# Performance work log

Measured on AMD Instinct MI355X. Metric: run time of the kernel, lower is better.

The kernel has to match this reference:

```python
import jax, jax.numpy as jnp
import numpy as np

T, TINI, N, P, M, B = 1500, 16, 32, 4, 4, 8192
LG = T - TINI - N + 1  # g dimension = 1453


def block_hankel(w, L, d):
    # w: flat signal of length T*d (row-major (T,d)); returns (L*d, T-L+1) block Hankel
    Tlen = w.shape[0] // d
    cols = Tlen - L + 1
    idx = jnp.arange(L * d)[:, None] + d * jnp.arange(cols)[None, :]
    return w[idx]


def setup_inputs():
    key = jax.random.key(0)
    ks = jax.random.split(key, 8)
    ud = jax.random.normal(ks[0], (T, M), jnp.float32)
    yd = jax.random.normal(ks[1], (T, P), jnp.float32)
    q = 100.0 + 0.01 * jax.random.normal(ks[2], (P,), jnp.float32)   # torch init: randn*0.01+100
    r = 0.01 + 0.001 * jax.random.normal(ks[3], (M,), jnp.float32)   # torch init: randn*0.001+0.01
    ref = jax.random.normal(ks[4], (B, N * P), jnp.float32)
    uref = jnp.zeros((B, N * M), jnp.float32)  # unused by forward math (matches torch)
    u_ini = jax.random.normal(ks[5], (B, TINI * M), jnp.float32)
    y_ini = jax.random.normal(ks[6], (B, TINI * P), jnp.float32)
    return dict(ref=ref, uref=uref, u_ini=u_ini, y_ini=y_ini, ud=ud, yd=yd, q=q, r=r)


def _forward(ref, u_ini, y_ini, ud, yd, q, r):
    # Hankel data matrices
    U = block_hankel(ud.reshape(-1), TINI + N, M)   # (M*(TINI+N), LG)
    Y = block_hankel(yd.reshape(-1), TINI + N, P)
    Up, Uf = U[: M * TINI], U[M * TINI :]           # (M*TINI, LG), (M*N, LG)
    Yp, Yf = Y[: P * TINI], Y[P * TINI :]

    # cost weights: Q_sqrt = diag(kron(ones(N), sqrt(q))) => squared weights tile(q, N)
    wq = jnp.tile(q, N)  # (N*P,)
    wr = jnp.tile(r, N)  # (N*M,)

    # QP in g: min g^T H g - 2 (Yf^T Wq ref)^T g  s.t.  A g = b
    H = Yf.T @ (wq[:, None] * Yf) + Uf.T @ (wr[:, None] * Uf)  # (LG, LG)
    A = jnp.concatenate([Up, Yp, Yf[-P:]], axis=0)             # equality constraints: Up g=u_ini, Yp g=y_ini, y[-P:]=ref[-P:]
    nc = A.shape[0]

    K = jnp.block([[2.0 * H, A.T], [A, jnp.zeros((nc, nc), H.dtype)]])  # KKT matrix (shared over batch)
    rhs = jnp.concatenate(
        [2.0 * (Yf.T @ (wq[:, None] * ref.T)), u_ini.T, y_ini.T, ref[:, -P:].T], axis=0
    )  # (LG+nc, B)

    sol = jnp.linalg.pinv(K) @ rhs   # min-norm KKT solution (K is singular: g non-unique, u/y unique)
    g = sol[:LG].T                   # (B, LG)
    u = g @ Uf.T                     # (B, N*M) optimal input
    y = g @ Yf.T                     # (B, N*P) optimal output
    return g, u, y


def reference(ref, uref, u_ini, y_ini, ud, yd, q, r):
    # uref is unused in the torch forward math as well (only a None-default placeholder)
    return _forward(ref, u_ini, y_ini, ud, yd, q, r)
```

## Files before the change

### kernel.cpp

```cpp
#include <hip/hip_runtime.h>

#define COLS_ 1453
#define NC 132
#define EGS 1792
#define NB 8192

#define oGam 0
#define oC   147456
#define oV   196608
#define oGC  213504
#define oCK  262656
#define oVK  311808
#define oGCK 328704
#define oB   377856
#define oP   410624
#define oR   414980
#define oJ   431364
#define oF   464132
#define oCE  496900

__device__ __forceinline__ double hash01(unsigned i, unsigned j) {
  unsigned x = i * 0x9E3779B9u ^ (j * 0x85EBCA6Bu + 0xC2B2AE35u);
  x ^= x >> 16; x *= 0x7FEB352Du; x ^= x >> 15; x *= 0x846CA68Bu; x ^= x >> 16;
  return (double)(x & 0xFFFFFF) / 8388608.0 - 1.0;
}

__global__ void k_gram(const float* __restrict__ ud, const float* __restrict__ yd,
                       double* __restrict__ G) {
  __shared__ float sig[12000];
  int tid = threadIdx.y * 16 + threadIdx.x;
  for (int idx = tid; idx < 6000; idx += 256) { sig[idx] = ud[idx]; sig[6000 + idx] = yd[idx]; }
  __syncthreads();
  int i = blockIdx.y * 16 + threadIdx.y;
  int j = blockIdx.x * 16 + threadIdx.x;
  const float* si = &sig[(i < 192) ? i : (6000 + i - 192)];
  const float* sj = &sig[(j < 192) ? j : (6000 + j - 192)];
  double a0 = 0.0, a1 = 0.0, a2 = 0.0, a3 = 0.0;
  for (int c = 0; c < 1452; c += 4) {
    a0 += (double)si[4 * c]      * (double)sj[4 * c];
    a1 += (double)si[4 * c + 4]  * (double)sj[4 * c + 4];
    a2 += (double)si[4 * c + 8]  * (double)sj[4 * c + 8];
    a3 += (double)si[4 * c + 12] * (double)sj[4 * c + 12];
  }
  a0 += (double)si[4 * 1452] * (double)sj[4 * 1452];
  G[i * 384 + j] = (a0 + a1) + (a2 + a3);
}

__global__ void k_initc(double* __restrict__ c, double* __restrict__ v) {
  int z = blockIdx.x * 16 + threadIdx.x;
  int i = blockIdx.y * 16 + threadIdx.y;
  if (i < 384) c[i * 128 + z] = hash01(i, z);
  else if (i < 516) v[(i - 384) * 128 + z] = hash01(i + 1000, z);
}

__global__ void k_G(const double* __restrict__ Gam, const double* __restrict__ c,
                    double* __restrict__ outp) {
  int z = blockIdx.x * 16 + threadIdx.x;
  int i = blockIdx.y * 16 + threadIdx.y;
  double a0 = 0.0, a1 = 0.0;
  for (int t = 0; t < 384; t += 2) {
    a0 += Gam[i * 384 + t]     * c[t * 128 + z];
    a1 += Gam[i * 384 + t + 1] * c[(t + 1) * 128 + z];
  }
  outp[i * 128 + z] = a0 + a1;
}

__global__ void k_step(const double* __restrict__ GC, const double* __restrict__ v,
                       const float* __restrict__ q, const float* __restrict__ r,
                       double* __restrict__ cK, double* __restrict__ vK) {
  int z = blockIdx.x * 16 + threadIdx.x;
  int i = blockIdx.y * 16 + threadIdx.y;
  if (i >= 516) return;
  if (i < 384) {
    double val;
    if (i < 64)        val = v[i * 128 + z];
    else if (i < 192)  { int m = i - 64;  val = 2.0 * (double)r[m & 3] * GC[i * 128 + z]; }
    else if (i < 256)  val = v[(64 + i - 192) * 128 + z];
    else {
      int m = i - 256;
      val = 2.0 * (double)q[m & 3] * GC[i * 128 + z];
      if (m >= 124) val += v[(128 + m - 124) * 128 + z];
    }
    cK[i * 128 + z] = val;
  } else {
    int rr = i - 384;
    double val;
    if (rr < 64)       val = GC[rr * 128 + z];
    else if (rr < 128) val = GC[(192 + rr - 64) * 128 + z];
    else               val = GC[(380 + rr - 128) * 128 + z];
    vK[rr * 128 + z] = val;
  }
}

__global__ void k_normc(double* __restrict__ c, double* __restrict__ v, double* __restrict__ GC) {
  __shared__ double red[256];
  int z = blockIdx.x, tid = threadIdx.x;
  double s = 0.0;
  for (int i = tid; i < 384; i += 256) s += c[i * 128 + z] * GC[i * 128 + z];
  for (int rr = tid; rr < 132; rr += 256) { double t = v[rr * 128 + z]; s += t * t; }
  red[tid] = s; __syncthreads();
  for (int st = 128; st > 0; st >>= 1) { if (tid < st) red[tid] += red[tid + st]; __syncthreads(); }
  double inv = rsqrt(red[0]);
  for (int i = tid; i < 384; i += 256) { c[i * 128 + z] *= inv; GC[i * 128 + z] *= inv; }
  for (int rr = tid; rr < 132; rr += 256) v[rr * 128 + z] *= inv;
}

__global__ void k_B(const double* __restrict__ c, const double* __restrict__ GCK,
                    const double* __restrict__ v, const double* __restrict__ vK,
                    double* __restrict__ Baug) {
  int z2 = blockIdx.x * 16 + threadIdx.x;
  int z1 = blockIdx.y * 16 + threadIdx.y;
  if (z2 >= 128) { Baug[z1 * 256 + z2] = ((z2 - 128) == z1) ? 1.0 : 0.0; return; }
  double a0 = 0.0, a1 = 0.0;
  for (int i = 0; i < 384; i += 2) {
    a0 += c[i * 128 + z1] * GCK[i * 128 + z2];
    a1 += c[(i + 1) * 128 + z1] * GCK[(i + 1) * 128 + z2];
  }
  for (int rr = 0; rr < 132; ++rr) a0 += v[rr * 128 + z1] * vK[rr * 128 + z2];
  Baug[z1 * 256 + z2] = a0 + a1;
}

__global__ __launch_bounds__(512) void k_inv(const double* __restrict__ src, int srcStride,
                                             double* __restrict__ dst, int n) {
  (void)n;
  __shared__ double pr[2][64];
  __shared__ double ckb[2][64];
  const int tid = threadIdx.x;
  const int r  = tid >> 3;
  const int cg = tid & 7;
  double a[8];
#pragma unroll
  for (int jj = 0; jj < 8; ++jj) a[jj] = src[r * srcStride + jj * 8 + cg];
#pragma unroll 1
  for (int k = 0; k < 64; ++k) {
    const int par = k & 1;
    const int ke = k & 7;
    const int kj = k >> 3;
    if (r == k) {
#pragma unroll
      for (int jj = 0; jj < 8; ++jj) pr[par][jj * 8 + cg] = a[jj];
    }
    if (cg == ke) {
#pragma unroll
      for (int jj = 0; jj < 8; ++jj) if (jj == kj) ckb[par][r] = a[jj];
    }
    __syncthreads();
    double pv  = 1.0 / pr[par][k];
    double fik = ckb[par][r];
    bool  isk  = (r == k);
    double f   = fik * pv;
    double fp  = isk ? (1.0 - pv) : f;
#pragma unroll
    for (int jj = 0; jj < 8; ++jj) a[jj] -= fp * pr[par][jj * 8 + cg];
    if (cg == ke) {
#pragma unroll
      for (int jj = 0; jj < 8; ++jj) if (jj == kj) a[jj] = isk ? pv : -f;
    }
  }
#pragma unroll
  for (int jj = 0; jj < 8; ++jj) dst[r * 64 + jj * 8 + cg] = a[jj];
}

__global__ void k_rowscale(const double* __restrict__ Maug, const double* __restrict__ P,
                           double* __restrict__ R, int stride, int nb, int k) {
  int c = nb * (k + 1) + blockIdx.x * 64 + threadIdx.x;
  if (c >= stride) return;
  int rr = blockIdx.y;
  double acc = 0.0;
  for (int t = 0; t < nb; ++t) acc += P[rr * nb + t] * Maug[(nb * k + t) * stride + c];
  R[rr * stride + c] = acc;
}

__global__ void k_update(double* __restrict__ Maug, const double* __restrict__ R,
                         int stride, int n, int nb, int k) {
  int c = nb * (k + 1) + blockIdx.x * 64 + threadIdx.x;
  if (c >= stride) return;
  int i = blockIdx.y;
  int ib = i - nb * k;
  if (ib >= 0 && ib < nb) { Maug[i * stride + c] = R[ib * stride + c]; return; }
  double acc = Maug[i * stride + c];
  for (int t = 0; t < nb; ++t) acc -= Maug[i * stride + nb * k + t] * R[t * stride + c];
  Maug[i * stride + c] = acc;
}

__global__ void k_J(const double* __restrict__ GC, const double* __restrict__ v,
                    const float* __restrict__ q, double* __restrict__ J) {
  int t = blockIdx.x * 16 + threadIdx.x;
  int z = blockIdx.y * 16 + threadIdx.y;
  double val;
  if (t < 128) {
    val = 2.0 * (double)q[t & 3] * GC[(256 + t) * 128 + z];
    if (t >= 124) val += v[(128 + t - 124) * 128 + z];
  } else if (t < 192) {
    val = v[(t - 128) * 128 + z];
  } else {
    val = v[(64 + t - 192) * 128 + z];
  }
  J[z * 256 + t] = val;
}

__global__ void k_F(const double* __restrict__ Baug, const double* __restrict__ J,
                    double* __restrict__ F) {
  int t = blockIdx.x * 16 + threadIdx.x;
  int z = blockIdx.y * 16 + threadIdx.y;
  double a0 = 0.0, a1 = 0.0;
  for (int w = 0; w < 128; w += 2) {
    a0 += Baug[z * 256 + 128 + w] * J[w * 256 + t];
    a1 += Baug[z * 256 + 128 + w + 1] * J[(w + 1) * 256 + t];
  }
  F[z * 256 + t] = a0 + a1;
}

__global__ void k_CE(const double* __restrict__ c, const double* __restrict__ F,
                     double* __restrict__ CE) {
  int t = blockIdx.x * 16 + threadIdx.x;
  int i = blockIdx.y * 16 + threadIdx.y;
  double a0 = 0.0, a1 = 0.0;
  for (int z = 0; z < 128; z += 2) {
    a0 += c[i * 128 + z] * F[z * 256 + t];
    a1 += c[i * 128 + z + 1] * F[(z + 1) * 256 + t];
  }
  CE[i * 256 + t] = a0 + a1;
}

__global__ void k_Egt(const double* __restrict__ CE, const float* __restrict__ ud,
                      const float* __restrict__ yd, float* __restrict__ Egt) {
  __shared__ float sig[12000];
  int tid = threadIdx.y * 16 + threadIdx.x;
  for (int idx = tid; idx < 6000; idx += 256) { sig[idx] = ud[idx]; sig[6000 + idx] = yd[idx]; }
  __syncthreads();
  int c = blockIdx.x * 16 + threadIdx.x;
  int t = blockIdx.y * 16 + threadIdx.y;
  double a0 = 0.0, a1 = 0.0;
  if (c < COLS_) {
    for (int i = 0; i < 384; i += 2) {
      int off0 = (i < 192) ? i : (6000 + i - 192);
      int off1 = (i + 1 < 192) ? (i + 1) : (6000 + i + 1 - 192);
      a0 += CE[i * 256 + t] * (double)sig[off0 + 4 * c];
      a1 += CE[(i + 1) * 256 + t] * (double)sig[off1 + 4 * c];
    }
  }
  Egt[t * EGS + c] = (float)(a0 + a1);
}

__global__ void k_Euy(const double* __restrict__ GC, const double* __restrict__ F,
                      float* __restrict__ Egt) {
  int n = blockIdx.x * 16 + threadIdx.x;
  int t = blockIdx.y * 16 + threadIdx.y;
  int row = (n < 128) ? (64 + n) : (128 + n);
  double a0 = 0.0, a1 = 0.0;
  for (int z = 0; z < 128; z += 2) {
    a0 += GC[row * 128 + z] * F[z * 256 + t];
    a1 += GC[row * 128 + z + 1] * F[(z + 1) * 256 + t];
  }
  Egt[t * EGS + 1536 + n] = (float)(a0 + a1);
}

__device__ __forceinline__ float4 loadA4(const float* __restrict__ ref, const float* __restrict__ ui,
                                         const float* __restrict__ yi, int m, int j) {
  if (j < 128) return *(const float4*)&ref[m * 128 + j];
  if (j < 192) return *(const float4*)&ui[m * 64 + (j - 128)];
  return *(const float4*)&yi[m * 64 + (j - 192)];
}

__global__ __launch_bounds__(256) void k_gemm1(const float* __restrict__ ref, const float* __restrict__ ui,
                                               const float* __restrict__ yi, const float* __restrict__ Bm,
                                               float* __restrict__ gout, float* __restrict__ uout,
                                               float* __restrict__ yout) {
  __shared__ float As[16 * 132];
  __shared__ float Bs[16 * 132];
  const int tid = threadIdx.x;
  const int m0 = blockIdx.y * 128;
  const int n0 = blockIdx.x * 128;
  const int tm  = (tid >> 4) * 8;
  const int tn0 = (tid & 15) * 4;
  const int aRow = tid >> 2;
  const int aQ   = (tid & 3) * 4;
  const int bK   = tid >> 5;
  const int bN   = (tid & 31) * 4;
  float acc[8][8] = {};
  for (int k0 = 0; k0 < 256; k0 += 16) {
    float4 av0 = loadA4(ref, ui, yi, m0 + aRow, k0 + aQ);
    float4 av1 = loadA4(ref, ui, yi, m0 + aRow + 64, k0 + aQ);
    float4 bv0 = *(const float4*)&Bm[(k0 + bK) * EGS + n0 + bN];
    float4 bv1 = *(const float4*)&Bm[(k0 + bK + 8) * EGS + n0 + bN];
    __syncthreads();
    As[(aQ + 0) * 132 + aRow] = av0.x;  As[(aQ + 1) * 132 + aRow] = av0.y;
    As[(aQ + 2) * 132 + aRow] = av0.z;  As[(aQ + 3) * 132 + aRow] = av0.w;
    As[(aQ + 0) * 132 + aRow + 64] = av1.x;  As[(aQ + 1) * 132 + aRow + 64] = av1.y;
    As[(aQ + 2) * 132 + aRow + 64] = av1.z;  As[(aQ + 3) * 132 + aRow + 64] = av1.w;
    *(float4*)&Bs[bK * 132 + bN] = bv0;
    *(float4*)&Bs[(bK + 8) * 132 + bN] = bv1;
    __syncthreads();
#pragma unroll
    for (int kk = 0; kk < 16; ++kk) {
      float4 a0 = *(const float4*)&As[kk * 132 + tm];
      float4 a1 = *(const float4*)&As[kk * 132 + tm + 4];
      float4 b0 = *(const float4*)&Bs[kk * 132 + tn0];
      float4 b1 = *(const float4*)&Bs[kk * 132 + 64 + tn0];
      float av[8] = {a0.x, a0.y, a0.z, a0.w, a1.x, a1.y, a1.z, a1.w};
      float bv[8] = {b0.x, b0.y, b0.z, b0.w, b1.x, b1.y, b1.z, b1.w};
#pragma unroll
      for (int i = 0; i < 8; ++i)
#pragma unroll
        for (int j = 0; j < 8; ++j) acc[i][j] += av[i] * bv[j];
    }
  }
#pragma unroll
  for (int i = 0; i < 8; ++i) {
    int m = m0 + tm + i;
#pragma unroll
    for (int j = 0; j < 8; ++j) {
      int n = n0 + ((j < 4) ? (tn0 + j) : (64 + tn0 + (j - 4)));
      float vv = acc[i][j];
      if (n < COLS_)       gout[(size_t)m * COLS_ + n] = vv;
      else if (n >= 1664)  yout[m * 128 + (n - 1664)] = vv;
      else if (n >= 1536)  uout[m * 128 + (n - 1536)] = vv;
    }
  }
}

extern "C" void kernel_launch(void* const* d_in, const int* in_sizes, int n_in,
                              void* d_out, int out_size, void* d_ws, size_t ws_size,
                              hipStream_t stream) {
  (void)in_sizes; (void)n_in; (void)out_size; (void)ws_size;
  const float* ref   = (const float*)d_in[0];
  const float* u_ini = (const float*)d_in[2];
  const float* y_ini = (const float*)d_in[3];
  const float* ud    = (const float*)d_in[4];
  const float* yd    = (const float*)d_in[5];
  const float* q     = (const float*)d_in[6];
  const float* r     = (const float*)d_in[7];

  float* out  = (float*)d_out;
  float* gout = out;
  float* uout = out + (size_t)NB * COLS_;
  float* yout = uout + (size_t)NB * 128;

  double* Wd  = (double*)d_out;
  double* Gam = Wd + oGam;
  double* c   = Wd + oC;
  double* v   = Wd + oV;
  double* GC  = Wd + oGC;
  double* cK  = Wd + oCK;
  double* vK  = Wd + oVK;
  double* GCK = Wd + oGCK;
  double* Ba  = Wd + oB;
  double* P   = Wd + oP;
  double* R   = Wd + oR;
  double* J   = Wd + oJ;
  double* F   = Wd + oF;
  double* CE  = Wd + oCE;
  float* Egt  = (float*)d_ws;

  k_gram<<<dim3(24, 24), dim3(16, 16), 0, stream>>>(ud, yd, Gam);

  k_initc<<<dim3(8, 33), dim3(16, 16), 0, stream>>>(c, v);
  double* ca = c;  double* va = v;
  double* cb = cK; double* vb = vK;
  for (int it = 0; it < 4; ++it) {
    k_G<<<dim3(8, 24), dim3(16, 16), 0, stream>>>(Gam, ca, GC);
    k_step<<<dim3(8, 33), dim3(16, 16), 0, stream>>>(GC, va, q, r, cb, vb);
    double* t1 = ca; ca = cb; cb = t1;
    double* t2 = va; va = vb; vb = t2;
  }

  k_G<<<dim3(8, 24), dim3(16, 16), 0, stream>>>(Gam, ca, GC);
  k_normc<<<128, 256, 0, stream>>>(ca, va, GC);
  k_step<<<dim3(8, 33), dim3(16, 16), 0, stream>>>(GC, va, q, r, cb, vb);
  k_G<<<dim3(8, 24), dim3(16, 16), 0, stream>>>(Gam, cb, GCK);
  k_B<<<dim3(16, 8), dim3(16, 16), 0, stream>>>(ca, GCK, va, vb, Ba);

  for (int k = 0; k < 2; ++k) {
    k_inv<<<1, 512, 0, stream>>>(Ba + (size_t)(64 * k) * 256 + 64 * k, 256, P, 64);
    int cs = 64 * (k + 1);
    int gx = (256 - cs + 63) / 64;
    k_rowscale<<<dim3(gx, 64), 64, 0, stream>>>(Ba, P, R, 256, 64, k);
    k_update<<<dim3(gx, 128), 64, 0, stream>>>(Ba, R, 256, 64, 64, k);
  }

  k_J<<<dim3(16, 8), dim3(16, 16), 0, stream>>>(GC, va, q, J);
  k_F<<<dim3(16, 8), dim3(16, 16), 0, stream>>>(Ba, J, F);
  k_CE<<<dim3(16, 24), dim3(16, 16), 0, stream>>>(ca, F, CE);
  k_Egt<<<dim3(96, 16), dim3(16, 16), 0, stream>>>(CE, ud, yd, Egt);
  k_Euy<<<dim3(16, 16), dim3(16, 16), 0, stream>>>(GC, F, Egt);

  k_gemm1<<<dim3(14, 64), dim3(256), 0, stream>>>(ref, u_ini, y_ini, Egt, gout, uout, yout);
}
```

Measured before the change: 647.3 us.

## Use split-bf16 MFMA (3-term) for final batched GEMM instead of FP32 FMA

New measurement: 587.7 us. 1.1x faster.

```diff
diff --git a/kernel.cpp b/kernel.cpp
--- a/kernel.cpp
+++ b/kernel.cpp
@@ -19,10 +19,22 @@
 #define oF   464132
 #define oCE  496900
 
+typedef short v8s __attribute__((ext_vector_type(8)));
+typedef float v4f __attribute__((ext_vector_type(4)));
+
 __device__ __forceinline__ double hash01(unsigned i, unsigned j) {
   unsigned x = i * 0x9E3779B9u ^ (j * 0x85EBCA6Bu + 0xC2B2AE35u);
   x ^= x >> 16; x *= 0x7FEB352Du; x ^= x >> 15; x *= 0x846CA68Bu; x ^= x >> 16;
   return (double)(x & 0xFFFFFF) / 8388608.0 - 1.0;
+}
+
+__device__ __forceinline__ unsigned short f2bf(float x) {
+  union { float f; unsigned u; } v; v.f = x;
+  unsigned r = (v.u + 0x7FFFu + ((v.u >> 16) & 1u)) >> 16;
+  return (unsigned short)r;
+}
+__device__ __forceinline__ float bf2f(unsigned short h) {
+  union { unsigned u; float f; } v; v.u = ((unsigned)h) << 16; return v.f;
 }
 
 __global__ void k_gram(const float* __restrict__ ud, const float* __restrict__ yd,
@@ -224,7 +236,8 @@
 }
 
 __global__ void k_Egt(const double* __restrict__ CE, const float* __restrict__ ud,
-                      const float* __restrict__ yd, float* __restrict__ Egt) {
+                      const float* __restrict__ yd, unsigned short* __restrict__ Eh,
+                      unsigned short* __restrict__ El) {
   __shared__ float sig[12000];
   int tid = threadIdx.y * 16 + threadIdx.x;
   for (int idx = tid; idx < 6000; idx += 256) { sig[idx] = ud[idx]; sig[6000 + idx] = yd[idx]; }
@@ -240,11 +253,16 @@
       a1 += CE[(i + 1) * 256 + t] * (double)sig[off1 + 4 * c];
     }
   }
-  Egt[t * EGS + c] = (float)(a0 + a1);
+  double s = a0 + a1;
+  float f = (float)s;
+  unsigned short h = f2bf(f);
+  float lo = (float)(s - (double)bf2f(h));
+  Eh[t * EGS + c] = h;
+  El[t * EGS + c] = f2bf(lo);
 }
 
 __global__ void k_Euy(const double* __restrict__ GC, const double* __restrict__ F,
-                      float* __restrict__ Egt) {
+                      unsigned short* __restrict__ Eh, unsigned short* __restrict__ El) {
   int n = blockIdx.x * 16 + threadIdx.x;
   int t = blockIdx.y * 16 + threadIdx.y;
   int row = (n < 128) ? (64 + n) : (128 + n);
@@ -253,7 +271,12 @@
     a0 += GC[row * 128 + z] * F[z * 256 + t];
     a1 += GC[row * 128 + z + 1] * F[(z + 1) * 256 + t];
   }
-  Egt[t * EGS + 1536 + n] = (float)(a0 + a1);
+  double s = a0 + a1;
+  float f = (float)s;
+  unsigned short h = f2bf(f);
+  float lo = (float)(s - (double)bf2f(h));
+  Eh[t * EGS + 1536 + n] = h;
+  El[t * EGS + 1536 + n] = f2bf(lo);
 }
 
 __device__ __forceinline__ float4 loadA4(const float* __restrict__ ref, const float* __restrict__ ui,
@@ -263,59 +286,113 @@
   return *(const float4*)&yi[m * 64 + (j - 192)];
 }
 
-__global__ __launch_bounds__(256) void k_gemm1(const float* __restrict__ ref, const float* __restrict__ ui,
-                                               const float* __restrict__ yi, const float* __restrict__ Bm,
-                                               float* __restrict__ gout, float* __restrict__ uout,
-                                               float* __restrict__ yout) {
-  __shared__ float As[16 * 132];
-  __shared__ float Bs[16 * 132];
+__global__ __launch_bounds__(256, 2) void k_gemm1(const float* __restrict__ ref, const float* __restrict__ ui,
+                                                  const float* __restrict__ yi,
+                                                  const unsigned short* __restrict__ Eh,
+                                                  const unsigned short* __restrict__ El,
+                                                  float* __restrict__ gout, float* __restrict__ uout,
+                                                  float* __restrict__ yout) {
+  __shared__ unsigned short Ah[128 * 32];
+  __shared__ unsigned short Al[128 * 32];
+  __shared__ unsigned short Bh[128 * 32];
+  __shared__ unsigned short Bl[128 * 32];
   const int tid = threadIdx.x;
   const int m0 = blockIdx.y * 128;
   const int n0 = blockIdx.x * 128;
-  const int tm  = (tid >> 4) * 8;
-  const int tn0 = (tid & 15) * 4;
-  const int aRow = tid >> 2;
-  const int aQ   = (tid & 3) * 4;
-  const int bK   = tid >> 5;
-  const int bN   = (tid & 31) * 4;
-  float acc[8][8] = {};
-  for (int k0 = 0; k0 < 256; k0 += 16) {
-    float4 av0 = loadA4(ref, ui, yi, m0 + aRow, k0 + aQ);
-    float4 av1 = loadA4(ref, ui, yi, m0 + aRow + 64, k0 + aQ);
-    float4 bv0 = *(const float4*)&Bm[(k0 + bK) * EGS + n0 + bN];
-    float4 bv1 = *(const float4*)&Bm[(k0 + bK + 8) * EGS + n0 + bN];
+  const int w  = tid >> 6;
+  const int lane = tid & 63;
+  const int wm = (w >> 1) * 64;
+  const int wn = (w & 1) * 64;
+  const int fr = lane & 15;
+  const int kg = lane >> 4;
+  const int sRow = tid & 127;
+  const int sKh  = tid >> 7;
+  const int sXor = (sRow >> 1) & 3;
+
+  v4f acc[4][4];
+#pragma unroll
+  for (int i = 0; i < 4; ++i)
+#pragma unroll
+    for (int j = 0; j < 4; ++j) acc[i][j] = (v4f){0.0f, 0.0f, 0.0f, 0.0f};
+
+  for (int k0 = 0; k0 < 256; k0 += 32) {
+    const int jb = k0 + sKh * 16;
+    float4 q0 = loadA4(ref, ui, yi, m0 + sRow, jb + 0);
+    float4 q1 = loadA4(ref, ui, yi, m0 + sRow, jb + 4);
+    float4 q2 = loadA4(ref, ui, yi, m0 + sRow, jb + 8);
+    float4 q3 = loadA4(ref, ui, yi, m0 + sRow, jb + 12);
+    unsigned short eh[16], el[16];
+#pragma unroll
+    for (int e = 0; e < 16; ++e) {
+      int idx = (jb + e) * EGS + n0 + sRow;
+      eh[e] = Eh[idx];
+      el[e] = El[idx];
+    }
     __syncthreads();
-    As[(aQ + 0) * 132 + aRow] = av0.x;  As[(aQ + 1) * 132 + aRow] = av0.y;
-    As[(aQ + 2) * 132 + aRow] = av0.z;  As[(aQ + 3) * 132 + aRow] = av0.w;
-    As[(aQ + 0) * 132 + aRow + 64] = av1.x;  As[(aQ + 1) * 132 + aRow + 64] = av1.y;
-    As[(aQ + 2) * 132 + aRow + 64] = av1.z;  As[(aQ + 3) * 132 + aRow + 64] = av1.w;
-    *(float4*)&Bs[bK * 132 + bN] = bv0;
-    *(float4*)&Bs[(bK + 8) * 132 + bN] = bv1;
+    float xa[16] = {q0.x, q0.y, q0.z, q0.w, q1.x, q1.y, q1.z, q1.w,
+                    q2.x, q2.y, q2.z, q2.w, q3.x, q3.y, q3.z, q3.w};
+    v8s ah0, ah1, al0, al1, bh0, bh1, bl0, bl1;
+#pragma unroll
+    for (int e = 0; e < 8; ++e) {
+      unsigned short h0 = f2bf(xa[e]);
+      ah0[e] = (short)h0;
+      al0[e] = (short)f2bf(xa[e] - bf2f(h0));
+      unsigned short h1 = f2bf(xa[8 + e]);
+      ah1[e] = (short)h1;
+      al1[e] = (short)f2bf(xa[8 + e] - bf2f(h1));
+      bh0[e] = (short)eh[e];
+      bh1[e] = (short)eh[8 + e];
+      bl0[e] = (short)el[e];
+      bl1[e] = (short)el[8 + e];
+    }
+    {
+      const int s0 = ((sKh * 2 + 0) ^ sXor) * 8;
+      const int s1 = ((sKh * 2 + 1) ^ sXor) * 8;
+      *(v8s*)&Ah[sRow * 32 + s0] = ah0;
+      *(v8s*)&Ah[sRow * 32 + s1] = ah1;
+      *(v8s*)&Al[sRow * 32 + s0] = al0;
+      *(v8s*)&Al[sRow * 32 + s1] = al1;
+      *(v8s*)&Bh[sRow * 32 + s0] = bh0;
+      *(v8s*)&Bh[sRow * 32 + s1] = bh1;
+      *(v8s*)&Bl[sRow * 32 + s0] = bl0;
+      *(v8s*)&Bl[sRow * 32 + s1] = bl1;
+    }
     __syncthreads();
-#pragma unroll
-    for (int kk = 0; kk < 16; ++kk) {
-      float4 a0 = *(const float4*)&As[kk * 132 + tm];
-      float4 a1 = *(const float4*)&As[kk * 132 + tm + 4];
-      float4 b0 = *(const float4*)&Bs[kk * 132 + tn0];
-      float4 b1 = *(const float4*)&Bs[kk * 132 + 64 + tn0];
-      float av[8] = {a0.x, a0.y, a0.z, a0.w, a1.x, a1.y, a1.z, a1.w};
-      float bv[8] = {b0.x, b0.y, b0.z, b0.w, b1.x, b1.y, b1.z, b1.w};
-#pragma unroll
-      for (int i = 0; i < 8; ++i)
-#pragma unroll
-        for (int j = 0; j < 8; ++j) acc[i][j] += av[i] * bv[j];
-    }
-  }
-#pragma unroll
-  for (int i = 0; i < 8; ++i) {
-    int m = m0 + tm + i;
-#pragma unroll
-    for (int j = 0; j < 8; ++j) {
-      int n = n0 + ((j < 4) ? (tn0 + j) : (64 + tn0 + (j - 4)));
-      float vv = acc[i][j];
-      if (n < COLS_)       gout[(size_t)m * COLS_ + n] = vv;
-      else if (n >= 1664)  yout[m * 128 + (n - 1664)] = vv;
-      else if (n >= 1536)  uout[m * 128 + (n - 1536)] = vv;
+    v8s fah[4], fal[4], fbh[4], fbl[4];
+#pragma unroll
+    for (int t4 = 0; t4 < 4; ++t4) {
+      int ar = wm + t4 * 16 + fr;
+      int as = (kg ^ ((ar >> 1) & 3)) * 8;
+      fah[t4] = *(const v8s*)&Ah[ar * 32 + as];
+      fal[t4] = *(const v8s*)&Al[ar * 32 + as];
+      int bc = wn + t4 * 16 + fr;
+      int bs = (kg ^ ((bc >> 1) & 3)) * 8;
+      fbh[t4] = *(const v8s*)&Bh[bc * 32 + bs];
+      fbl[t4] = *(const v8s*)&Bl[bc * 32 + bs];
+    }
+#pragma unroll
+    for (int tm = 0; tm < 4; ++tm)
+#pragma unroll
+      for (int tn = 0; tn < 4; ++tn) {
+        acc[tm][tn] = __builtin_amdgcn_mfma_f32_16x16x32_bf16(fal[tm], fbh[tn], acc[tm][tn], 0, 0, 0);
+        acc[tm][tn] = __builtin_amdgcn_mfma_f32_16x16x32_bf16(fah[tm], fbl[tn], acc[tm][tn], 0, 0, 0);
+        acc[tm][tn] = __builtin_amdgcn_mfma_f32_16x16x32_bf16(fah[tm], fbh[tn], acc[tm][tn], 0, 0, 0);
+      }
+  }
+#pragma unroll
+  for (int tm = 0; tm < 4; ++tm) {
+    const int mb = m0 + wm + tm * 16 + kg * 4;
+#pragma unroll
+    for (int tn = 0; tn < 4; ++tn) {
+      const int n = n0 + wn + tn * 16 + fr;
+#pragma unroll
+      for (int r = 0; r < 4; ++r) {
+        float vv = acc[tm][tn][r];
+        int m = mb + r;
+        if (n < COLS_)       gout[(size_t)m * COLS_ + n] = vv;
+        else if (n >= 1664)  yout[m * 128 + (n - 1664)] = vv;
+        else if (n >= 1536)  uout[m * 128 + (n - 1536)] = vv;
+      }
     }
   }
 }
@@ -351,7 +428,8 @@
   double* J   = Wd + oJ;
   double* F   = Wd + oF;
   double* CE  = Wd + oCE;
-  float* Egt  = (float*)d_ws;
+  unsigned short* Eh = (unsigned short*)d_ws;
+  unsigned short* El = Eh + (size_t)256 * EGS;
 
   k_gram<<<dim3(24, 24), dim3(16, 16), 0, stream>>>(ud, yd, Gam);
 
@@ -382,8 +460,8 @@
   k_J<<<dim3(16, 8), dim3(16, 16), 0, stream>>>(GC, va, q, J);
   k_F<<<dim3(16, 8), dim3(16, 16), 0, stream>>>(Ba, J, F);
   k_CE<<<dim3(16, 24), dim3(16, 16), 0, stream>>>(ca, F, CE);
-  k_Egt<<<dim3(96, 16), dim3(16, 16), 0, stream>>>(CE, ud, yd, Egt);
-  k_Euy<<<dim3(16, 16), dim3(16, 16), 0, stream>>>(GC, F, Egt);
-
-  k_gemm1<<<dim3(14, 64), dim3(256), 0, stream>>>(ref, u_ini, y_ini, Egt, gout, uout, yout);
-}
+  k_Egt<<<dim3(96, 16), dim3(16, 16), 0, stream>>>(CE, ud, yd, Eh, El);
+  k_Euy<<<dim3(16, 16), dim3(16, 16), 0, stream>>>(GC, F, Eh, El);
+
+  k_gemm1<<<dim3(14, 64), dim3(256), 0, stream>>>(ref, u_ini, y_ini, Eh, El, gout, uout, yout);
+}
```
